# Kernel optimization log

Hardware: AMD Instinct MI355X
Metric: run time of the kernel (lower is better)

Reference implementation:

```python
import jax, jax.numpy as jnp
import numpy as np

B, S, D = 2, 2048, 2048
NQ, NKV = 16, 4
HD = D // NQ           # 128
GROUP = NQ // NKV      # 4


def setup_inputs() -> dict:
    key = jax.random.key(0)
    k_x, k_q, k_k, k_v, k_o = jax.random.split(key, 5)
    scale = 0.02
    return {
        "x": jax.random.normal(k_x, (B, S, D), dtype=jnp.float32),
        # torch nn.Linear weights have shape (out_features, in_features)
        "Wq": jax.random.normal(k_q, (D, D), dtype=jnp.float32) * scale,
        "Wk": jax.random.normal(k_k, (NKV * HD, D), dtype=jnp.float32) * scale,
        "Wv": jax.random.normal(k_v, (NKV * HD, D), dtype=jnp.float32) * scale,
        "Wo": jax.random.normal(k_o, (D, D), dtype=jnp.float32) * scale,
    }


def reference(x, Wq, Wk, Wv, Wo):
    b, s, _ = x.shape
    # projections (Linear: x @ W.T), then split heads -> (b, h, s, hd)
    Q = (x @ Wq.T).reshape(b, s, NQ, HD).transpose(0, 2, 1, 3)
    K = (x @ Wk.T).reshape(b, s, NKV, HD).transpose(0, 2, 1, 3)
    V = (x @ Wv.T).reshape(b, s, NKV, HD).transpose(0, 2, 1, 3)
    # GQA: broadcast each KV head across its query-head group (repeat_interleave on head dim)
    K = jnp.repeat(K, GROUP, axis=1)  # (b, NQ, s, hd)
    V = jnp.repeat(V, GROUP, axis=1)
    scores = jnp.einsum("bhqd,bhkd->bhqk", Q, K) / jnp.sqrt(jnp.float32(HD))
    causal = jnp.triu(jnp.ones((s, s), dtype=bool), k=1)  # True above diagonal -> masked
    scores = jnp.where(causal, -jnp.inf, scores)
    weights = jax.nn.softmax(scores, axis=-1)  # dropout p=0.0 -> identity
    ctx = jnp.einsum("bhqk,bhkd->bhqd", weights, V)
    ctx = ctx.transpose(0, 2, 1, 3).reshape(b, s, D)
    return ctx @ Wo.T
```

## Files before the change

### kernel.cpp

```cpp
#include <hip/hip_runtime.h>
#include <stdint.h>

#define S_LEN 2048
#define DMODEL 2048
#define NQH 16
#define NKVH 4
#define HDK 128

typedef __bf16 bf16x8 __attribute__((ext_vector_type(8)));
typedef float f32x4 __attribute__((ext_vector_type(4)));
typedef float f32x16 __attribute__((ext_vector_type(16)));

__device__ __forceinline__ void async16(const void* g, void* l) {
  __builtin_amdgcn_global_load_lds((const __attribute__((address_space(1))) void*)g,
                                   (__attribute__((address_space(3))) void*)l,
                                   16, 0, 0);
}

__device__ __forceinline__ f32x4 mfma16(bf16x8 a, bf16x8 b, f32x4 c) {
  return __builtin_amdgcn_mfma_f32_16x16x32_bf16(a, b, c, 0, 0, 0);
}
__device__ __forceinline__ f32x16 mfma32(bf16x8 a, bf16x8 b, f32x16 c) {
  return __builtin_amdgcn_mfma_f32_32x32x16_bf16(a, b, c, 0, 0, 0);
}
__device__ __forceinline__ uint32_t pkbf16(float lo, float hi) {
  uint32_t r;
  asm("v_cvt_pk_bf16_f32 %0, %1, %2" : "=v"(r) : "v"(lo), "v"(hi));
  return r;
}

__global__ __launch_bounds__(256) void cvt_all(
    const float* __restrict__ i0, const float* __restrict__ i1,
    const float* __restrict__ i2, const float* __restrict__ i3,
    const float* __restrict__ i4, __bf16* __restrict__ o0,
    __bf16* __restrict__ o1, __bf16* __restrict__ o2, __bf16* __restrict__ o3,
    __bf16* __restrict__ o4) {
  int v = blockIdx.x * 256 + threadIdx.x;
  const float* in;
  __bf16* out;
  int base;
  if (v < 1048576)      { in = i0; out = o0; base = 0; }
  else if (v < 1572864) { in = i1; out = o1; base = 1048576; }
  else if (v < 1703936) { in = i2; out = o2; base = 1572864; }
  else if (v < 1835008) { in = i3; out = o3; base = 1703936; }
  else                  { in = i4; out = o4; base = 1835008; }
  int i = (v - base) * 8;
  const float4* p = (const float4*)(in + i);
  float4 a = p[0], b = p[1];
  bf16x8 o;
  o[0] = (__bf16)a.x; o[1] = (__bf16)a.y; o[2] = (__bf16)a.z; o[3] = (__bf16)a.w;
  o[4] = (__bf16)b.x; o[5] = (__bf16)b.y; o[6] = (__bf16)b.z; o[7] = (__bf16)b.w;
  *(bf16x8*)(out + i) = o;
}

template <bool F32OUT>
__global__ __launch_bounds__(256) void gemm_bt(const __bf16* __restrict__ A,
                                               const __bf16* __restrict__ B0,
                                               const __bf16* __restrict__ B1,
                                               const __bf16* __restrict__ B2,
                                               void* __restrict__ C0,
                                               void* __restrict__ C1,
                                               void* __restrict__ C2,
                                               int Ntot, int Ns1, int Ns2, int K) {
  int nbn = Ntot >> 7;
  int nwg = gridDim.x;
  int bid = blockIdx.x;
  int bx = (bid & 7) * (nwg >> 3) + (bid >> 3);
  int m0 = (bx / nbn) << 7;
  int n0g = (bx % nbn) << 7;
  const __bf16* B;
  void* C;
  int n0, Nc;
  if (n0g < Ns1)      { B = B0; C = C0; n0 = n0g;       Nc = Ns1; }
  else if (n0g < Ns2) { B = B1; C = C1; n0 = n0g - Ns1; Nc = Ns2 - Ns1; }
  else                { B = B2; C = C2; n0 = n0g - Ns2; Nc = Ntot - Ns2; }

  __shared__ __align__(16) uint8_t As[16384];
  __shared__ __align__(16) uint8_t Bs[16384];

  int t = threadIdx.x, lane = t & 63, w = t >> 6;
  int wr = w >> 1, wc = w & 1;
  f32x4 acc[4][4] = {};

  for (int k0 = 0; k0 < K; k0 += 64) {
#pragma unroll
    for (int i = 0; i < 4; ++i) {
      int c = (i << 8) + t;
      int row = c >> 3;
      int colb = ((c & 7) << 4) ^ ((row & 7) << 4);
      async16((const uint8_t*)(A + (size_t)(m0 + row) * K + k0) + colb, As + c * 16);
      async16((const uint8_t*)(B + (size_t)(n0 + row) * K + k0) + colb, Bs + c * 16);
    }
    __syncthreads();
#pragma unroll
    for (int ks = 0; ks < 2; ++ks) {
      bf16x8 af[4], bfr[4];
#pragma unroll
      for (int m = 0; m < 4; ++m) {
        int row = wr * 64 + m * 16 + (lane & 15);
        int colb = ((ks << 6) + ((lane >> 4) << 4)) ^ ((row & 7) << 4);
        af[m] = *(const bf16x8*)(As + row * 128 + colb);
      }
#pragma unroll
      for (int n = 0; n < 4; ++n) {
        int row = wc * 64 + n * 16 + (lane & 15);
        int colb = ((ks << 6) + ((lane >> 4) << 4)) ^ ((row & 7) << 4);
        bfr[n] = *(const bf16x8*)(Bs + row * 128 + colb);
      }
      __builtin_amdgcn_s_setprio(1);
#pragma unroll
      for (int m = 0; m < 4; ++m)
#pragma unroll
        for (int n = 0; n < 4; ++n)
          acc[m][n] = mfma16(af[m], bfr[n], acc[m][n]);
      __builtin_amdgcn_s_setprio(0);
    }
    __syncthreads();
  }
#pragma unroll
  for (int m = 0; m < 4; ++m)
#pragma unroll
    for (int n = 0; n < 4; ++n)
#pragma unroll
      for (int j = 0; j < 4; ++j) {
        int mg = m0 + wr * 64 + m * 16 + ((lane >> 4) << 2) + j;
        int ng = n0 + wc * 64 + n * 16 + (lane & 15);
        float v = acc[m][n][j];
        if (F32OUT) ((float*)C)[(size_t)mg * Nc + ng] = v;
        else        ((__bf16*)C)[(size_t)mg * Nc + ng] = (__bf16)v;
      }
}

__global__ __launch_bounds__(256) void transpose_v(const __bf16* __restrict__ V,
                                                   __bf16* __restrict__ Vt) {
  int bid = blockIdx.x;
  int dt = bid & 1, st = (bid >> 1) & 31, kvh = (bid >> 6) & 3, b = bid >> 8;
  __shared__ __align__(16) __bf16 tile[64][72];
  int t = threadIdx.x;
#pragma unroll
  for (int i = 0; i < 2; ++i) {
    int c = (i << 8) + t;
    int sr = c >> 3, cb = (c & 7) << 3;
    bf16x8 v = *(const bf16x8*)(V + (size_t)(b * S_LEN + st * 64 + sr) * 512 +
                                kvh * HDK + dt * 64 + cb);
    *(bf16x8*)(&tile[sr][cb]) = v;
  }
  __syncthreads();
  size_t tbase = ((size_t)(b * NKVH + kvh) * 32 + st) * 8192;
#pragma unroll
  for (int i = 0; i < 2; ++i) {
    int c = (i << 8) + t;
    int g = c & 15, dr0 = (c >> 4) << 1;
    bf16x8 o;
#pragma unroll
    for (int j = 0; j < 4; ++j) o[j] = tile[4 * g + j][dr0];
#pragma unroll
    for (int j = 0; j < 4; ++j) o[4 + j] = tile[4 * g + j][dr0 + 1];
    *(bf16x8*)(Vt + tbase + g * 512 + (size_t)(dt * 64 + dr0) * 4) = o;
  }
}

__global__ __launch_bounds__(256, 2) void attn(const __bf16* __restrict__ Q,
                                               const __bf16* __restrict__ Kx,
                                               const __bf16* __restrict__ Vt,
                                               __bf16* __restrict__ Ctx) {
  int bid0 = blockIdx.x;
  int bid = ((bid0 & 7) << 6) | (bid0 >> 3);
  int qt = 15 - (bid & 15);
  int h = (bid >> 4) & 15;
  int b = bid >> 8;
  int kvh = h >> 2;
  int q0 = qt << 7;
  int t = threadIdx.x, lane = t & 63, w = t >> 6;
  int qr = lane & 31;
  int hi = lane >> 5;
  int qwb = q0 + (w << 5);

  __shared__ __align__(16) uint8_t Ks[2][16384];
  __shared__ __align__(16) uint8_t Vs[2][16384];

  const __bf16* kbase = Kx + (size_t)b * S_LEN * 512 + kvh * HDK;
  const __bf16* vbase = Vt + (size_t)(b * NKVH + kvh) * 32 * 8192;

  auto stage = [&](int kt, int bufi) {
#pragma unroll
    for (int i = 0; i < 4; ++i) {
      int c = (i << 8) + t;
      int krow = c >> 4;
      int kcolb = ((c & 15) << 4) ^ ((krow & 7) << 4);
      async16((const uint8_t*)(kbase + (size_t)((kt << 6) + krow) * 512) + kcolb,
              Ks[bufi] + c * 16);
      async16((const uint8_t*)(vbase + (size_t)kt * 8192) + c * 16,
              Vs[bufi] + c * 16);
    }
  };

  int NT = (qt << 1) + 2;
  stage(0, 0);

  bf16x8 qf[8];
  {
    const __bf16* qrow = Q + (size_t)(b * S_LEN + qwb + qr) * DMODEL + h * HDK + hi * 8;
#pragma unroll
    for (int dk = 0; dk < 8; ++dk) qf[dk] = *(const bf16x8*)(qrow + dk * 16);
  }
  __syncthreads();

  const float NEG = -3.0e38f;
  const float SC = 0.08838834764831845f;
  float m_run = NEG, l_run = 0.f;
  f32x16 acc[4] = {};

  for (int kt = 0; kt < NT; ++kt) {
    int cur = kt & 1;
    if (kt + 1 < NT) stage(kt + 1, cur ^ 1);
    int k0 = kt << 6;
    if (k0 <= qwb + 31) {
      const uint8_t* ks = Ks[cur];
      const uint8_t* vs = Vs[cur];

      f32x16 st0 = {}, st1 = {};
      __builtin_amdgcn_s_setprio(1);
#pragma unroll
      for (int dk = 0; dk < 8; ++dk) {
        int cb = (dk << 5) + (hi << 4);
        int swz = (qr & 7) << 4;
        bf16x8 kf0 = *(const bf16x8*)(ks + qr * 256 + (cb ^ swz));
        st0 = mfma32(kf0, qf[dk], st0);
        bf16x8 kf1 = *(const bf16x8*)(ks + (32 + qr) * 256 + (cb ^ swz));
        st1 = mfma32(kf1, qf[dk], st1);
      }
      __builtin_amdgcn_s_setprio(0);

      if (k0 + 63 > qwb) {
#pragma unroll
        for (int r = 0; r < 16; ++r) {
          int kl = (r & 3) + ((r >> 2) << 3) + (hi << 2);
          st0[r] = (k0 + kl > qwb + qr) ? NEG : st0[r];
          st1[r] = (k0 + 32 + kl > qwb + qr) ? NEG : st1[r];
        }
      }

      float tm[16];
#pragma unroll
      for (int r = 0; r < 16; ++r) tm[r] = fmaxf(st0[r], st1[r]);
#pragma unroll
      for (int s = 8; s > 0; s >>= 1)
#pragma unroll
        for (int r = 0; r < s; ++r) tm[r] = fmaxf(tm[r], tm[r + s]);
      float mx = fmaxf(tm[0], __shfl_xor(tm[0], 32, 64));

      if (__any(mx > m_run + 90.52f)) {
        float mn = fmaxf(m_run, mx);
        float al = __expf((m_run - mn) * SC);
        l_run *= al;
        m_run = mn;
#pragma unroll
        for (int i = 0; i < 16; ++i) {
          float alr = __shfl(al, (i & 3) + ((i >> 2) << 3) + (hi << 2), 64);
          acc[0][i] *= alr; acc[1][i] *= alr; acc[2][i] *= alr; acc[3][i] *= alr;
        }
      }

      float mSC = m_run * SC;
      float p0[16], p1[16];
#pragma unroll
      for (int r = 0; r < 16; ++r) p0[r] = __expf(fmaf(st0[r], SC, -mSC));
#pragma unroll
      for (int r = 0; r < 16; ++r) p1[r] = __expf(fmaf(st1[r], SC, -mSC));
      float ts[16];
#pragma unroll
      for (int r = 0; r < 16; ++r) ts[r] = p0[r] + p1[r];
#pragma unroll
      for (int s = 8; s > 0; s >>= 1)
#pragma unroll
        for (int r = 0; r < s; ++r) ts[r] += ts[r + s];
      l_run += ts[0];

      bf16x8 pa[4];
      {
        union { bf16x8 v; uint32_t u[4]; } t0, t1, t2, t3;
#pragma unroll
        for (int i = 0; i < 4; ++i) {
          t0.u[i] = pkbf16(p0[2 * i], p0[2 * i + 1]);
          t1.u[i] = pkbf16(p0[8 + 2 * i], p0[9 + 2 * i]);
          t2.u[i] = pkbf16(p1[2 * i], p1[2 * i + 1]);
          t3.u[i] = pkbf16(p1[8 + 2 * i], p1[9 + 2 * i]);
        }
        pa[0] = t0.v; pa[1] = t1.v; pa[2] = t2.v; pa[3] = t3.v;
      }

      __builtin_amdgcn_s_setprio(1);
#pragma unroll
      for (int dt = 0; dt < 4; ++dt) {
        int row = (dt << 5) + qr;
#pragma unroll
        for (int kc = 0; kc < 4; ++kc) {
          int g0 = (kc << 2) + hi;
          union { bf16x8 v; uint64_t q[2]; } vfu;
          vfu.q[0] = *(const uint64_t*)(vs + (g0 << 10) + (row << 3));
          vfu.q[1] = *(const uint64_t*)(vs + ((g0 + 2) << 10) + (row << 3));
          acc[dt] = mfma32(pa[kc], vfu.v, acc[dt]);
        }
      }
      __builtin_amdgcn_s_setprio(0);
    }
    __syncthreads();
  }

  l_run += __shfl_xor(l_run, 32, 64);
#pragma unroll
  for (int i = 0; i < 16; ++i) {
    int rm = (i & 3) + ((i >> 2) << 3) + (hi << 2);
    float lr = __shfl(l_run, rm, 64);
    float inv = 1.0f / lr;
    size_t rowoff = (size_t)(b * S_LEN + qwb + rm) * DMODEL + h * HDK + qr;
#pragma unroll
    for (int dt = 0; dt < 4; ++dt)
      Ctx[rowoff + (dt << 5)] = (__bf16)(acc[dt][i] * inv);
  }
}

extern "C" void kernel_launch(void* const* d_in, const int* in_sizes, int n_in,
                              void* d_out, int out_size, void* d_ws, size_t ws_size,
                              hipStream_t stream) {
  const float* x  = (const float*)d_in[0];
  const float* Wq = (const float*)d_in[1];
  const float* Wk = (const float*)d_in[2];
  const float* Wv = (const float*)d_in[3];
  const float* Wo = (const float*)d_in[4];
  float* out = (float*)d_out;

  const size_t MB = 1024 * 1024;
  uint8_t* ws = (uint8_t*)d_ws;
  __bf16* xb  = (__bf16*)(ws + 0 * MB);
  __bf16* Wqb = (__bf16*)(ws + 16 * MB);
  __bf16* Wkb = (__bf16*)(ws + 24 * MB);
  __bf16* Wvb = (__bf16*)(ws + 26 * MB);
  __bf16* Wob = (__bf16*)(ws + 28 * MB);
  __bf16* Qb  = (__bf16*)(ws + 36 * MB);
  __bf16* Kb  = (__bf16*)(ws + 52 * MB);
  __bf16* Vb  = (__bf16*)(ws + 56 * MB);
  __bf16* Vtb = (__bf16*)(ws + 60 * MB);
  __bf16* Ctx = (__bf16*)(ws + 64 * MB);

  cvt_all<<<9216, 256, 0, stream>>>(x, Wq, Wk, Wv, Wo, xb, Wqb, Wkb, Wvb, Wob);

  gemm_bt<false><<<(4096 / 128) * (3072 / 128), 256, 0, stream>>>(
      xb, Wqb, Wkb, Wvb, (void*)Qb, (void*)Kb, (void*)Vb, 3072, 2048, 2560, 2048);

  transpose_v<<<512, 256, 0, stream>>>(Vb, Vtb);

  attn<<<512, 256, 0, stream>>>(Qb, Kb, Vtb, Ctx);

  gemm_bt<true><<<(4096 / 128) * (2048 / 128), 256, 0, stream>>>(
      Ctx, Wob, Wob, Wob, (void*)out, (void*)out, (void*)out, 2048, 2048, 2048, 2048);
}
```

Before: 194.1 us.

## Fuse V transpose into QKV GEMM epilogue and split QK^T accumulation chains

The QKV projection GEMM now writes the V segment straight into the tiled transposed layout that attention consumes, so the separate transpose_v kernel launch and the intermediate V buffer round trip are gone. The cost is scattered 2-byte stores for the V columns in the GEMM epilogue. Separately, the attention QK^T loop now splits the head dimension into two independent MFMA accumulator chains that are summed at the end. This is meant to hide MFMA dependency latency, at the price of extra accumulator registers in a kernel already bounded to two waves per SIMD.

```diff
diff --git a/kernel.cpp b/kernel.cpp
--- a/kernel.cpp
+++ b/kernel.cpp
@@ -53,7 +53,7 @@
   *(bf16x8*)(out + i) = o;
 }
 
-template <bool F32OUT>
+template <bool F32OUT, bool VSEG2>
 __global__ __launch_bounds__(256) void gemm_bt(const __bf16* __restrict__ A,
                                                const __bf16* __restrict__ B0,
                                                const __bf16* __restrict__ B1,
@@ -71,9 +71,10 @@
   const __bf16* B;
   void* C;
   int n0, Nc;
+  bool seg2 = false;
   if (n0g < Ns1)      { B = B0; C = C0; n0 = n0g;       Nc = Ns1; }
   else if (n0g < Ns2) { B = B1; C = C1; n0 = n0g - Ns1; Nc = Ns2 - Ns1; }
-  else                { B = B2; C = C2; n0 = n0g - Ns2; Nc = Ntot - Ns2; }
+  else                { B = B2; C = C2; n0 = n0g - Ns2; Nc = Ntot - Ns2; seg2 = true; }
 
   __shared__ __align__(16) uint8_t As[16384];
   __shared__ __align__(16) uint8_t Bs[16384];
@@ -126,38 +127,18 @@
         int mg = m0 + wr * 64 + m * 16 + ((lane >> 4) << 2) + j;
         int ng = n0 + wc * 64 + n * 16 + (lane & 15);
         float v = acc[m][n][j];
-        if (F32OUT) ((float*)C)[(size_t)mg * Nc + ng] = v;
-        else        ((__bf16*)C)[(size_t)mg * Nc + ng] = (__bf16)v;
-      }
-}
-
-__global__ __launch_bounds__(256) void transpose_v(const __bf16* __restrict__ V,
-                                                   __bf16* __restrict__ Vt) {
-  int bid = blockIdx.x;
-  int dt = bid & 1, st = (bid >> 1) & 31, kvh = (bid >> 6) & 3, b = bid >> 8;
-  __shared__ __align__(16) __bf16 tile[64][72];
-  int t = threadIdx.x;
-#pragma unroll
-  for (int i = 0; i < 2; ++i) {
-    int c = (i << 8) + t;
-    int sr = c >> 3, cb = (c & 7) << 3;
-    bf16x8 v = *(const bf16x8*)(V + (size_t)(b * S_LEN + st * 64 + sr) * 512 +
-                                kvh * HDK + dt * 64 + cb);
-    *(bf16x8*)(&tile[sr][cb]) = v;
-  }
-  __syncthreads();
-  size_t tbase = ((size_t)(b * NKVH + kvh) * 32 + st) * 8192;
-#pragma unroll
-  for (int i = 0; i < 2; ++i) {
-    int c = (i << 8) + t;
-    int g = c & 15, dr0 = (c >> 4) << 1;
-    bf16x8 o;
-#pragma unroll
-    for (int j = 0; j < 4; ++j) o[j] = tile[4 * g + j][dr0];
-#pragma unroll
-    for (int j = 0; j < 4; ++j) o[4 + j] = tile[4 * g + j][dr0 + 1];
-    *(bf16x8*)(Vt + tbase + g * 512 + (size_t)(dt * 64 + dr0) * 4) = o;
-  }
+        if (VSEG2 && seg2) {
+          int bb = mg >> 11, s = mg & 2047;
+          size_t vidx = ((size_t)((bb << 2) + (ng >> 7)) * 32 + (s >> 6)) * 8192 +
+                        (size_t)((s >> 2) & 15) * 512 + (size_t)(ng & 127) * 4 +
+                        (s & 3);
+          ((__bf16*)C)[vidx] = (__bf16)v;
+        } else if (F32OUT) {
+          ((float*)C)[(size_t)mg * Nc + ng] = v;
+        } else {
+          ((__bf16*)C)[(size_t)mg * Nc + ng] = (__bf16)v;
+        }
+      }
 }
 
 __global__ __launch_bounds__(256, 2) void attn(const __bf16* __restrict__ Q,
@@ -219,18 +200,25 @@
       const uint8_t* ks = Ks[cur];
       const uint8_t* vs = Vs[cur];
 
-      f32x16 st0 = {}, st1 = {};
+      f32x16 st0 = {}, st1 = {}, st0b = {}, st1b = {};
+      int swz = (qr & 7) << 4;
       __builtin_amdgcn_s_setprio(1);
 #pragma unroll
-      for (int dk = 0; dk < 8; ++dk) {
-        int cb = (dk << 5) + (hi << 4);
-        int swz = (qr & 7) << 4;
-        bf16x8 kf0 = *(const bf16x8*)(ks + qr * 256 + (cb ^ swz));
-        st0 = mfma32(kf0, qf[dk], st0);
-        bf16x8 kf1 = *(const bf16x8*)(ks + (32 + qr) * 256 + (cb ^ swz));
-        st1 = mfma32(kf1, qf[dk], st1);
+      for (int dk = 0; dk < 4; ++dk) {
+        int cb0 = (dk << 5) + (hi << 4);
+        int cb1 = ((dk + 4) << 5) + (hi << 4);
+        bf16x8 a0 = *(const bf16x8*)(ks + qr * 256 + (cb0 ^ swz));
+        bf16x8 a1 = *(const bf16x8*)(ks + (32 + qr) * 256 + (cb0 ^ swz));
+        bf16x8 b0 = *(const bf16x8*)(ks + qr * 256 + (cb1 ^ swz));
+        bf16x8 b1 = *(const bf16x8*)(ks + (32 + qr) * 256 + (cb1 ^ swz));
+        st0 = mfma32(a0, qf[dk], st0);
+        st1 = mfma32(a1, qf[dk], st1);
+        st0b = mfma32(b0, qf[dk + 4], st0b);
+        st1b = mfma32(b1, qf[dk + 4], st1b);
       }
       __builtin_amdgcn_s_setprio(0);
+      st0 = st0 + st0b;
+      st1 = st1 + st1b;
 
       if (k0 + 63 > qwb) {
 #pragma unroll
@@ -340,19 +328,16 @@
   __bf16* Wob = (__bf16*)(ws + 28 * MB);
   __bf16* Qb  = (__bf16*)(ws + 36 * MB);
   __bf16* Kb  = (__bf16*)(ws + 52 * MB);
-  __bf16* Vb  = (__bf16*)(ws + 56 * MB);
   __bf16* Vtb = (__bf16*)(ws + 60 * MB);
   __bf16* Ctx = (__bf16*)(ws + 64 * MB);
 
   cvt_all<<<9216, 256, 0, stream>>>(x, Wq, Wk, Wv, Wo, xb, Wqb, Wkb, Wvb, Wob);
 
-  gemm_bt<false><<<(4096 / 128) * (3072 / 128), 256, 0, stream>>>(
-      xb, Wqb, Wkb, Wvb, (void*)Qb, (void*)Kb, (void*)Vb, 3072, 2048, 2560, 2048);
-
-  transpose_v<<<512, 256, 0, stream>>>(Vb, Vtb);
+  gemm_bt<false, true><<<(4096 / 128) * (3072 / 128), 256, 0, stream>>>(
+      xb, Wqb, Wkb, Wvb, (void*)Qb, (void*)Kb, (void*)Vtb, 3072, 2048, 2560, 2048);
 
   attn<<<512, 256, 0, stream>>>(Qb, Kb, Vtb, Ctx);
 
-  gemm_bt<true><<<(4096 / 128) * (2048 / 128), 256, 0, stream>>>(
+  gemm_bt<true, false><<<(4096 / 128) * (2048 / 128), 256, 0, stream>>>(
       Ctx, Wob, Wob, Wob, (void*)out, (void*)out, (void*)out, 2048, 2048, 2048, 2048);
 }
```

New measurement: 193.9 us. Within noise of the previous version (-0.1%).
